# Performance work log

Hardware: AMD Instinct MI355X
Metric: run time of the kernel (lower is better)

The kernel has to match this reference:

```python
import jax, jax.numpy as jnp
from jax import lax
import numpy as np

N = 2000            # number of RPN proposals
NUM_CLASSES = 21    # Pascal-VOC classes (incl. background, as the original loops all classes)
MAX_PER_CLASS = 50
MAX_PER_IMAGE = 100
IOU_THR = 0.7
NEG = jnp.float32(-1e9)


def setup_inputs() -> dict:
    key = jax.random.key(0)
    k1, k2, k3, k4 = jax.random.split(key, 4)
    # valid [y1, x1, y2, x2] proposals inside a ~600x600 image
    yx = jax.random.uniform(k1, (N, 2), dtype=jnp.float32) * 600.0
    hw = jax.random.uniform(k2, (N, 2), dtype=jnp.float32) * 120.0 + 16.0
    rpn_proposals_bboxes = jnp.concatenate([yx, yx + hw], axis=1)
    roi_bboxes_txtytwth = jax.random.normal(k3, (N, 4), dtype=jnp.float32) * 0.1
    roi_score = jax.random.uniform(k4, (N, NUM_CLASSES), dtype=jnp.float32)
    return {
        "rpn_proposals_bboxes": rpn_proposals_bboxes,
        "roi_bboxes_txtytwth": roi_bboxes_txtytwth,
        "roi_score": roi_score,
    }


def _decode_bbox(props, deltas):
    h = props[:, 2] - props[:, 0]
    w = props[:, 3] - props[:, 1]
    cy = props[:, 0] + 0.5 * h
    cx = props[:, 1] + 0.5 * w
    dy, dx, dh, dw = deltas[:, 0], deltas[:, 1], deltas[:, 2], deltas[:, 3]
    pcy = dy * h + cy
    pcx = dx * w + cx
    ph = h * jnp.exp(dh)
    pw = w * jnp.exp(dw)
    return jnp.stack([pcy - 0.5 * ph, pcx - 0.5 * pw, pcy + 0.5 * ph, pcx + 0.5 * pw], axis=1)


def _pairwise_iou(boxes):
    # boxes: [N,4] -> iou [N,N]
    y1, x1, y2, x2 = boxes[:, 0], boxes[:, 1], boxes[:, 2], boxes[:, 3]
    area = (y2 - y1) * (x2 - x1)                      # [N]
    iy1 = jnp.maximum(y1[:, None], y1[None, :])
    ix1 = jnp.maximum(x1[:, None], x1[None, :])
    iy2 = jnp.minimum(y2[:, None], y2[None, :])
    ix2 = jnp.minimum(x2[:, None], x2[None, :])
    inter = jnp.maximum(iy2 - iy1, 0.0) * jnp.maximum(ix2 - ix1, 0.0)
    union = area[:, None] + area[None, :] - inter
    return inter / jnp.maximum(union, 1e-8)


def _nms_keep(iou_sorted):
    # iou_sorted: [N,N] IoU among boxes already sorted by descending score.
    # Greedy NMS: box i kept iff no earlier kept box overlaps it > IOU_THR.
    def body(kept, xs):
        row, i = xs                                    # row: iou of box i vs all
        suppressed = jnp.any(kept & (row > IOU_THR))
        kept = kept.at[i].set(~suppressed)
        return kept, None
    kept, _ = lax.scan(body, jnp.zeros((N,), dtype=bool), (iou_sorted, jnp.arange(N)))
    return kept


def reference(rpn_proposals_bboxes, roi_bboxes_txtytwth, roi_score):
    final_bboxes = _decode_bbox(rpn_proposals_bboxes, roi_bboxes_txtytwth)   # [N,4]
    iou = _pairwise_iou(final_bboxes)                                        # [N,N]

    # per-class descending score order
    order = jnp.argsort(-roi_score.T, axis=1)                                # [C,N]
    scores_sorted = jnp.take_along_axis(roi_score.T, order, axis=1)          # [C,N]
    # reorder IoU per class: [C,N,N]
    iou_sorted = jax.vmap(lambda o: iou[o][:, o])(order)
    kept = jax.vmap(_nms_keep)(iou_sorted)                                   # [C,N] bool
    # cap at MAX_PER_CLASS kept boxes per class (NMS max_output_size)
    rank = jnp.cumsum(kept.astype(jnp.int32), axis=1)
    valid = kept & (rank <= MAX_PER_CLASS)
    masked_scores = jnp.where(valid, scores_sorted, NEG)                     # [C,N]

    boxes_sorted = final_bboxes[order]                                       # [C,N,4]
    cls_ids = jnp.broadcast_to(jnp.arange(NUM_CLASSES, dtype=jnp.int32)[:, None], (NUM_CLASSES, N))

    # global top-k over all surviving (class, box) pairs
    flat_scores = masked_scores.reshape(-1)                                  # [C*N]
    _, idx = lax.top_k(flat_scores, MAX_PER_IMAGE)
    out_bboxes = boxes_sorted.reshape(-1, 4)[idx]                            # [K,4]
    out_cls = cls_ids.reshape(-1)[idx]                                       # [K]
    return out_bboxes, out_cls
```

## Files before the change

### kernel.cpp

```cpp
#include <hip/hip_runtime.h>

#define N 2000
#define NCLS 21
#define MAXPC 50
#define MAXPI 100
#define IOU_THR 0.7f

typedef unsigned long long u64;
typedef unsigned int u32;

__device__ __forceinline__ u32 sortable(float s) {
    u32 u = __float_as_uint(s);
    return ((int)u < 0) ? ~u : (u | 0x80000000u);
}

__device__ __forceinline__ float4 decode_one(const float* __restrict__ rpn,
                                             const float* __restrict__ deltas, int i) {
    float4 p = ((const float4*)rpn)[i];
    float4 d = ((const float4*)deltas)[i];
    float h = p.z - p.x, w = p.w - p.y;
    float cy = p.x + 0.5f * h, cx = p.y + 0.5f * w;
    float pcy = d.x * h + cy;
    float pcx = d.y * w + cx;
    float ph = h * expf(d.z);
    float pw = w * expf(d.w);
    return make_float4(pcy - 0.5f * ph, pcx - 0.5f * pw, pcy + 0.5f * ph, pcx + 0.5f * pw);
}

__device__ __forceinline__ float iou_vs(float4 b, float ar,
                                        float kx, float ky, float kz, float kw) {
    float ka = (kz - kx) * (kw - ky);
    float iy1 = fmaxf(b.x, kx), ix1 = fmaxf(b.y, ky);
    float iy2 = fminf(b.z, kz), ix2 = fminf(b.w, kw);
    float inter = fmaxf(iy2 - iy1, 0.f) * fmaxf(ix2 - ix1, 0.f);
    return inter / fmaxf(ar + ka - inter, 1e-8f);
}

__global__ void sort_kernel(const float* __restrict__ score, int* __restrict__ order) {
    __shared__ __align__(16) u64 skey[N];
    int c = blockIdx.x;
    for (int i = threadIdx.x; i < N; i += blockDim.x) {
        u32 u = sortable(score[i * NCLS + c]);
        skey[i] = ((u64)u << 32) | (u32)(~i);
    }
    __syncthreads();
    int i = blockIdx.y * 64 + (threadIdx.x >> 2);
    int q = threadIdx.x & 3;
    if (i < N) {
        u64 ki = skey[i];
        const ulonglong2* s2 = (const ulonglong2*)skey;
        int r = 0;
        int jj0 = q * 250;
#pragma unroll 4
        for (int jj = jj0; jj < jj0 + 250; jj++) {
            ulonglong2 v = s2[jj];
            r += (v.x > ki);
            r += (v.y > ki);
        }
        r += __shfl_xor(r, 1);
        r += __shfl_xor(r, 2);
        if (q == 0) order[c * N + r] = i;
    }
}

__global__ void nms_kernel(const float* __restrict__ rpn,
                           const float* __restrict__ deltas,
                           const int* __restrict__ order,
                           const float* __restrict__ score,
                           int* __restrict__ keep_pos,
                           int* __restrict__ keep_cnt,
                           u64* __restrict__ cand_key) {
    __shared__ float4 cbox[64];
    __shared__ float4 kbox[MAXPC];
    int c = blockIdx.x;
    int lane = threadIdx.x;
    int nk = 0;
    const int NCH = (N + 63) / 64;
    for (int chunk = 0; chunk < NCH && nk < MAXPC; chunk++) {
        int pos = chunk * 64 + lane;
        bool valid = pos < N;
        int oi = order[c * N + (valid ? pos : (N - 1))];
        float4 bb = decode_one(rpn, deltas, oi);
        cbox[lane] = bb;
        float ar = (bb.z - bb.x) * (bb.w - bb.y);
        bool sup = !valid;
        for (int k = 0; k < nk; k++) {
            float4 kb = kbox[k];
            sup = sup || (iou_vs(bb, ar, kb.x, kb.y, kb.z, kb.w) > IOU_THR);
        }
        u64 supby = 0;
#pragma unroll 4
        for (int j = 0; j < 64; j++) {
            float4 bj = cbox[j];
            supby |= (u64)(iou_vs(bb, ar, bj.x, bj.y, bj.z, bj.w) > IOU_THR) << j;
        }
        u64 alive = __ballot(!sup);
        for (int l = 0; l < 64 && nk < MAXPC; l++) {
            u64 col = __ballot((supby >> l) & 1);
            if ((alive >> l) & 1) {
                if (lane == l) {
                    kbox[nk] = bb;
                    keep_pos[c * MAXPC + nk] = pos;
                    u32 u = sortable(score[oi * NCLS + c]);
                    cand_key[c * MAXPC + nk] = ((u64)u << 32) | (u32)(~(c * N + pos));
                }
                nk++;
                alive &= ~(col & (~0ull << (l + 1)));
            }
        }
    }
    if (lane == 0) keep_cnt[c] = nk;
}

__global__ void __launch_bounds__(1024, 1)
topk_kernel(const float* __restrict__ rpn, const float* __restrict__ deltas,
            const int* __restrict__ order,
            const int* __restrict__ keep_pos, const int* __restrict__ keep_cnt,
            const u64* __restrict__ cand_key,
            float* __restrict__ out) {
    __shared__ u64 tk[NCLS * MAXPC];
    __shared__ int scnt[NCLS];
    int tid = threadIdx.x;
    for (int t = tid; t < NCLS * MAXPC; t += 1024)
        tk[t] = cand_key[t];
    if (tid < NCLS) scnt[tid] = keep_cnt[tid];
    __syncthreads();
    int M = 0;
#pragma unroll
    for (int c2 = 0; c2 < NCLS; c2++) M += scnt[c2];

    for (int t = tid; t < NCLS * MAXPC; t += 1024) {
        int cc = t / MAXPC, k = t - cc * MAXPC;
        if (k >= scnt[cc]) continue;
        u64 ki = tk[t];
        int r = k;
#pragma unroll
        for (int c2 = 0; c2 < NCLS; c2++) {
            if (c2 == cc) continue;
            int lo = 0, hi = scnt[c2];
            while (lo < hi) {
                int mid = (lo + hi) >> 1;
                if (tk[c2 * MAXPC + mid] > ki) lo = mid + 1; else hi = mid;
            }
            r += lo;
        }
        if (r < MAXPI) {
            int flat = (int)(~(u32)ki);
            int pos = flat - cc * N;
            int oi = order[cc * N + pos];
            float4 bb = decode_one(rpn, deltas, oi);
            out[r * 4 + 0] = bb.x;
            out[r * 4 + 1] = bb.y;
            out[r * 4 + 2] = bb.z;
            out[r * 4 + 3] = bb.w;
            out[4 * MAXPI + r] = (float)cc;
        }
    }
    if (tid == 0 && M < MAXPI) {
        int m = M;
        int cnt0 = scnt[0];
        for (int pos = 0; pos < 150 && m < MAXPI; pos++) {
            bool validp = false;
            for (int k = 0; k < cnt0; k++)
                if (keep_pos[k] == pos) { validp = true; break; }
            if (!validp) {
                int oi = order[pos];
                float4 bb = decode_one(rpn, deltas, oi);
                out[m * 4 + 0] = bb.x;
                out[m * 4 + 1] = bb.y;
                out[m * 4 + 2] = bb.z;
                out[m * 4 + 3] = bb.w;
                out[4 * MAXPI + m] = 0.0f;
                m++;
            }
        }
    }
}

extern "C" void kernel_launch(void* const* d_in, const int* in_sizes, int n_in,
                              void* d_out, int out_size, void* d_ws, size_t ws_size,
                              hipStream_t stream) {
    const float* rpn    = (const float*)d_in[0];
    const float* deltas = (const float*)d_in[1];
    const float* score  = (const float*)d_in[2];
    float* out = (float*)d_out;

    char* ws = (char*)d_ws;
    int*   order    = (int*)(ws);
    u64*   candk    = (u64*)(ws + 168000);
    int*   keep_pos = (int*)(ws + 176400);
    int*   keep_cnt = (int*)(ws + 180600);

    sort_kernel<<<dim3(NCLS, 32), 256, 0, stream>>>(score, order);
    nms_kernel<<<NCLS, 64, 0, stream>>>(rpn, deltas, order, score,
                                        keep_pos, keep_cnt, candk);
    topk_kernel<<<1, 1024, 0, stream>>>(rpn, deltas, order,
                                        keep_pos, keep_cnt, candk, out);
}
```

Measured before the change: 53.76 us.

## Fuse per-class NMS and global top-k into a single-block kernel

```diff
diff --git a/kernel.cpp b/kernel.cpp
--- a/kernel.cpp
+++ b/kernel.cpp
@@ -63,68 +63,58 @@
     }
 }
 
-__global__ void nms_kernel(const float* __restrict__ rpn,
-                           const float* __restrict__ deltas,
-                           const int* __restrict__ order,
-                           const float* __restrict__ score,
-                           int* __restrict__ keep_pos,
-                           int* __restrict__ keep_cnt,
-                           u64* __restrict__ cand_key) {
-    __shared__ float4 cbox[64];
-    __shared__ float4 kbox[MAXPC];
-    int c = blockIdx.x;
-    int lane = threadIdx.x;
-    int nk = 0;
-    const int NCH = (N + 63) / 64;
-    for (int chunk = 0; chunk < NCH && nk < MAXPC; chunk++) {
-        int pos = chunk * 64 + lane;
-        bool valid = pos < N;
-        int oi = order[c * N + (valid ? pos : (N - 1))];
-        float4 bb = decode_one(rpn, deltas, oi);
-        cbox[lane] = bb;
-        float ar = (bb.z - bb.x) * (bb.w - bb.y);
-        bool sup = !valid;
-        for (int k = 0; k < nk; k++) {
-            float4 kb = kbox[k];
-            sup = sup || (iou_vs(bb, ar, kb.x, kb.y, kb.z, kb.w) > IOU_THR);
-        }
-        u64 supby = 0;
+__global__ void __launch_bounds__(1024, 1)
+nms_topk_kernel(const float* __restrict__ rpn, const float* __restrict__ deltas,
+                const float* __restrict__ score,
+                const int* __restrict__ order,
+                float* __restrict__ out) {
+    __shared__ float4 kbox[NCLS][MAXPC];
+    __shared__ float4 cbox[16][64];
+    __shared__ u64 candk[NCLS][MAXPC];
+    __shared__ int scnt[NCLS];
+
+    int tid = threadIdx.x;
+    int w = tid >> 6, lane = tid & 63;
+
+    for (int cls = w; cls < NCLS; cls += 16) {
+        int nk = 0;
+        const int NCH = (N + 63) / 64;
+        for (int chunk = 0; chunk < NCH && nk < MAXPC; chunk++) {
+            int pos = chunk * 64 + lane;
+            bool valid = pos < N;
+            int oi = order[cls * N + (valid ? pos : (N - 1))];
+            float4 bb = decode_one(rpn, deltas, oi);
+            cbox[w][lane] = bb;
+            float ar = (bb.z - bb.x) * (bb.w - bb.y);
+            bool sup = !valid;
+            for (int k = 0; k < nk; k++) {
+                float4 kb = kbox[cls][k];
+                sup = sup || (iou_vs(bb, ar, kb.x, kb.y, kb.z, kb.w) > IOU_THR);
+            }
+            u64 supby = 0;
 #pragma unroll 4
-        for (int j = 0; j < 64; j++) {
-            float4 bj = cbox[j];
-            supby |= (u64)(iou_vs(bb, ar, bj.x, bj.y, bj.z, bj.w) > IOU_THR) << j;
-        }
-        u64 alive = __ballot(!sup);
-        for (int l = 0; l < 64 && nk < MAXPC; l++) {
-            u64 col = __ballot((supby >> l) & 1);
-            if ((alive >> l) & 1) {
-                if (lane == l) {
-                    kbox[nk] = bb;
-                    keep_pos[c * MAXPC + nk] = pos;
-                    u32 u = sortable(score[oi * NCLS + c]);
-                    cand_key[c * MAXPC + nk] = ((u64)u << 32) | (u32)(~(c * N + pos));
+            for (int j = 0; j < 64; j++) {
+                float4 bj = cbox[w][j];
+                supby |= (u64)(iou_vs(bb, ar, bj.x, bj.y, bj.z, bj.w) > IOU_THR) << j;
+            }
+            u64 alive = __ballot(!sup);
+            for (int l = 0; l < 64 && nk < MAXPC; l++) {
+                u64 col = __ballot((supby >> l) & 1);
+                if ((alive >> l) & 1) {
+                    if (lane == l) {
+                        kbox[cls][nk] = bb;
+                        u32 u = sortable(score[oi * NCLS + cls]);
+                        candk[cls][nk] = ((u64)u << 32) | (u32)(~(cls * N + pos));
+                    }
+                    nk++;
+                    alive &= ~(col & (~0ull << (l + 1)));
                 }
-                nk++;
-                alive &= ~(col & (~0ull << (l + 1)));
             }
         }
+        if (lane == 0) scnt[cls] = nk;
     }
-    if (lane == 0) keep_cnt[c] = nk;
-}
+    __syncthreads();
 
-__global__ void __launch_bounds__(1024, 1)
-topk_kernel(const float* __restrict__ rpn, const float* __restrict__ deltas,
-            const int* __restrict__ order,
-            const int* __restrict__ keep_pos, const int* __restrict__ keep_cnt,
-            const u64* __restrict__ cand_key,
-            float* __restrict__ out) {
-    __shared__ u64 tk[NCLS * MAXPC];
-    __shared__ int scnt[NCLS];
-    int tid = threadIdx.x;
-    for (int t = tid; t < NCLS * MAXPC; t += 1024)
-        tk[t] = cand_key[t];
-    if (tid < NCLS) scnt[tid] = keep_cnt[tid];
-    __syncthreads();
     int M = 0;
 #pragma unroll
     for (int c2 = 0; c2 < NCLS; c2++) M += scnt[c2];
@@ -132,7 +122,7 @@
     for (int t = tid; t < NCLS * MAXPC; t += 1024) {
         int cc = t / MAXPC, k = t - cc * MAXPC;
         if (k >= scnt[cc]) continue;
-        u64 ki = tk[t];
+        u64 ki = candk[cc][k];
         int r = k;
 #pragma unroll
         for (int c2 = 0; c2 < NCLS; c2++) {
@@ -140,7 +130,7 @@
             int lo = 0, hi = scnt[c2];
             while (lo < hi) {
                 int mid = (lo + hi) >> 1;
-                if (tk[c2 * MAXPC + mid] > ki) lo = mid + 1; else hi = mid;
+                if (candk[c2][mid] > ki) lo = mid + 1; else hi = mid;
             }
             r += lo;
         }
@@ -160,10 +150,10 @@
         int m = M;
         int cnt0 = scnt[0];
         for (int pos = 0; pos < 150 && m < MAXPI; pos++) {
-            bool validp = false;
+            bool kept = false;
             for (int k = 0; k < cnt0; k++)
-                if (keep_pos[k] == pos) { validp = true; break; }
-            if (!validp) {
+                if ((int)(~(u32)candk[0][k]) == pos) { kept = true; break; }
+            if (!kept) {
                 int oi = order[pos];
                 float4 bb = decode_one(rpn, deltas, oi);
                 out[m * 4 + 0] = bb.x;
@@ -185,15 +175,8 @@
     const float* score  = (const float*)d_in[2];
     float* out = (float*)d_out;
 
-    char* ws = (char*)d_ws;
-    int*   order    = (int*)(ws);
-    u64*   candk    = (u64*)(ws + 168000);
-    int*   keep_pos = (int*)(ws + 176400);
-    int*   keep_cnt = (int*)(ws + 180600);
+    int* order = (int*)d_ws;
 
     sort_kernel<<<dim3(NCLS, 32), 256, 0, stream>>>(score, order);
-    nms_kernel<<<NCLS, 64, 0, stream>>>(rpn, deltas, order, score,
-                                        keep_pos, keep_cnt, candk);
-    topk_kernel<<<1, 1024, 0, stream>>>(rpn, deltas, order,
-                                        keep_pos, keep_cnt, candk, out);
+    nms_topk_kernel<<<1, 1024, 0, stream>>>(rpn, deltas, score, order, out);
 }
```

Result: slower. 71.43 us (+32.9%).
